# Kernel optimization log

Measured on AMD Instinct MI355X. Metric: run time of the kernel, lower is better.

## Reference

```python
import jax, jax.numpy as jnp
import numpy as np

E, N, F = 50000, 25000, 32

def setup_inputs() -> dict:
    key = jax.random.key(0)
    ks = jax.random.split(key, 8)
    efeat = jax.random.normal(ks[0], (E, F), dtype=jnp.float32) * 0.2
    initial_efeats = jax.random.normal(ks[1], (E, F), dtype=jnp.float32) * 0.2
    # msg_fn / attn_fn: Linear(F, F*F)
    Wm = jax.random.normal(ks[2], (F * F, F), dtype=jnp.float32) * 0.05
    bm = jnp.zeros((F * F,), dtype=jnp.float32)
    Wa = jax.random.normal(ks[3], (F * F, F), dtype=jnp.float32) * 0.05
    ba = jnp.zeros((F * F,), dtype=jnp.float32)
    src = jax.random.randint(ks[4], (E,), 0, N, dtype=jnp.int32)
    dst = jax.random.randint(ks[5], (E,), 0, N, dtype=jnp.int32)
    return {"efeat": efeat, "initial_efeats": initial_efeats, "Wm": Wm, "bm": bm,
            "Wa": Wa, "ba": ba, "src": src, "dst": dst, "num_nodes": N}

def reference(efeat, initial_efeats, Wm, bm, Wa, ba, src, dst, num_nodes):
    e, f = efeat.shape
    # edge-conditioned transform matrices: [E, F, F]
    w_m = (efeat @ Wm.T + bm).reshape(e, f, f)
    w_a = (efeat @ Wa.T + ba).reshape(e, f, f)
    h = efeat[:, :, None]                 # [E, F, 1]
    ih = initial_efeats[:, :, None]       # [E, F, 1]
    e1 = w_m * h                          # [E, F, F]
    exp_e2 = jnp.exp(w_a * h)             # [E, F, F]
    initial_e1 = w_m * ih
    exp_initial_e2 = jnp.exp(w_a * ih)
    # scatter-sum exp weights to destination nodes, gather back at src
    sum_exp_node = jax.ops.segment_sum(exp_e2, dst, num_segments=num_nodes)  # [N, F, F]
    sum_exp = sum_exp_node[src] - exp_e2 + exp_initial_e2
    h1 = exp_e2 * e1
    initial_h1 = exp_initial_e2 * initial_e1
    m_node = jax.ops.segment_sum(h1, dst, num_segments=num_nodes)            # [N, F, F]
    h2 = (m_node[src] - h1 + initial_h1) / sum_exp
    return h2.sum(axis=1)                 # [E, F]
```

## Files before the change

kernel.cpp:

```cpp
#include <hip/hip_runtime.h>
#include <hip/hip_fp16.h>
#include <math.h>
#include <stdint.h>


#define FDIM   32
#define NNODES 25000
#define NPB    8

typedef __attribute__((ext_vector_type(8))) short bf16x8;
typedef __attribute__((ext_vector_type(4))) float f32x4;

__device__ __forceinline__ unsigned short f2bf(float f) {
    unsigned u = __float_as_uint(f);
    return (unsigned short)((u + 0x7FFFu + ((u >> 16) & 1u)) >> 16);
}
__device__ __forceinline__ unsigned f2e5(float f) {
    unsigned short hb = __half_as_ushort(__float2half(f));
    return (unsigned)((unsigned short)((hb + 0x7Fu + ((hb >> 8) & 1u)) >> 8)) & 0xFFu;
}
__device__ __forceinline__ float e52f(unsigned b) {
    return __half2float(__ushort_as_half((unsigned short)(b << 8)));
}

__global__ __launch_bounds__(256) void zero_f4(float4* __restrict__ p, int n4) {
    int i = blockIdx.x * blockDim.x + threadIdx.x;
    int stride = gridDim.x * blockDim.x;
    float4 z = make_float4(0.f, 0.f, 0.f, 0.f);
    for (; i < n4; i += stride) p[i] = z;
}

__global__ __launch_bounds__(256) void k_hist(
    const int* __restrict__ src, const int* __restrict__ dst,
    int* __restrict__ cnt_src, int* __restrict__ cnt_dst, int E) {
    int e = blockIdx.x * blockDim.x + threadIdx.x;
    if (e < E) {
        atomicAdd(&cnt_dst[dst[e]], 1);
        atomicAdd(&cnt_src[src[e]], 1);
    }
}

__global__ __launch_bounds__(256) void k_scan2(
    const int* __restrict__ cnt_dst, int* __restrict__ off_dst, int* __restrict__ cur_dst,
    const int* __restrict__ cnt_src, int* __restrict__ off_src, int* __restrict__ cur_src,
    int n) {
    const int* cnt = blockIdx.x ? cnt_src : cnt_dst;
    int* off = blockIdx.x ? off_src : off_dst;
    int* cur = blockIdx.x ? cur_src : cur_dst;
    __shared__ int wsum[4];
    __shared__ int carry_sh;
    const int tid = threadIdx.x, lane = tid & 63, w = tid >> 6;
    if (tid == 0) carry_sh = 0;
    __syncthreads();
    for (int base = 0; base < n; base += 1024) {
        int i0 = base + tid * 4;
        int v0 = (i0 + 0 < n) ? cnt[i0 + 0] : 0;
        int v1 = (i0 + 1 < n) ? cnt[i0 + 1] : 0;
        int v2 = (i0 + 2 < n) ? cnt[i0 + 2] : 0;
        int v3 = (i0 + 3 < n) ? cnt[i0 + 3] : 0;
        int s = v0 + v1 + v2 + v3;
        int inc = s;
        for (int d = 1; d < 64; d <<= 1) {
            int t = __shfl_up(inc, d, 64);
            if (lane >= d) inc += t;
        }
        if (lane == 63) wsum[w] = inc;
        __syncthreads();
        int wbase = 0;
        for (int k = 0; k < w; ++k) wbase += wsum[k];
        int carry = carry_sh;
        int excl = carry + wbase + inc - s;
        if (i0 + 0 < n) { off[i0 + 0] = excl; cur[i0 + 0] = excl; } excl += v0;
        if (i0 + 1 < n) { off[i0 + 1] = excl; cur[i0 + 1] = excl; } excl += v1;
        if (i0 + 2 < n) { off[i0 + 2] = excl; cur[i0 + 2] = excl; } excl += v2;
        if (i0 + 3 < n) { off[i0 + 3] = excl; cur[i0 + 3] = excl; }
        __syncthreads();
        if (tid == 255) carry_sh = carry + wbase + inc;
    }
    __syncthreads();
    if (tid == 0) off[n] = carry_sh;
}

__global__ __launch_bounds__(256) void k_scatter(
    const int* __restrict__ src, const int* __restrict__ dst,
    int* __restrict__ cur_src, int* __restrict__ cur_dst,
    int* __restrict__ eb_src, int* __restrict__ eb_dst, int E) {
    int e = blockIdx.x * blockDim.x + threadIdx.x;
    if (e < E) {
        int p = atomicAdd(&cur_dst[dst[e]], 1); eb_dst[p] = e;
        int q = atomicAdd(&cur_src[src[e]], 1); eb_src[q] = e;
    }
}

__global__ __launch_bounds__(256) void prep_w(
    const float* __restrict__ Wm, const float* __restrict__ Wa,
    short* __restrict__ wbuf) {
    int idx = blockIdx.x * blockDim.x + threadIdx.x;
    if (idx >= 2 * 64 * 64) return;
    int mat  = idx >> 12;
    int jt   = (idx >> 6) & 63;
    int lane = idx & 63;
    const float* W = mat ? Wa : Wm;
    const float* s = W + (size_t)(jt * 16 + (lane & 15)) * FDIM + (lane >> 4) * 8;
    bf16x8 v;
#pragma unroll
    for (int t = 0; t < 8; ++t) v[t] = (short)f2bf(s[t]);
    *(bf16x8*)(wbuf + (size_t)idx * 8) = v;
}

__global__ __launch_bounds__(256) void gemm(
    const float* __restrict__ efeat,
    const float* __restrict__ bm, const float* __restrict__ ba,
    const short* __restrict__ wbuf,
    unsigned short* __restrict__ buf, int E)
{
    const int lane = threadIdx.x & 63;
    const int wid  = threadIdx.x >> 6;
    const int et   = blockIdx.x * 4 + wid;
    if (et * 16 >= E) return;
    const int r16 = lane & 15;
    const int kq  = lane >> 4;

    const float* xa = efeat + (size_t)(et * 16 + r16) * FDIM + kq * 8;
    bf16x8 afrag;
#pragma unroll
    for (int t = 0; t < 8; ++t) afrag[t] = (short)f2bf(xa[t]);

    for (int jt = 0; jt < 64; ++jt) {
        bf16x8 bfm = *(const bf16x8*)(wbuf + ((size_t)(jt)      * 64 + lane) * 8);
        bf16x8 bfa = *(const bf16x8*)(wbuf + ((size_t)(64 + jt) * 64 + lane) * 8);
        const int j = jt * 16 + r16;
        const float biasm = bm[j], biasa = ba[j];
        f32x4 accm = {biasm, biasm, biasm, biasm};
        f32x4 acca = {biasa, biasa, biasa, biasa};
        accm = __builtin_amdgcn_mfma_f32_16x16x32_bf16(afrag, bfm, accm, 0, 0, 0);
        acca = __builtin_amdgcn_mfma_f32_16x16x32_bf16(afrag, bfa, acca, 0, 0, 0);
#pragma unroll
        for (int r = 0; r < 4; ++r) {
            int e = et * 16 + kq * 4 + r;
            unsigned pk = f2e5(accm[r]) | (f2e5(acca[r]) << 8);
            buf[(size_t)e * 1024 + j] = (unsigned short)pk;
        }
    }
}

__global__ __launch_bounds__(256) void consume(
    const float* __restrict__ efeat, const float* __restrict__ ifeat,
    const unsigned short* __restrict__ buf,
    const int* __restrict__ off_dst, const int* __restrict__ eb_dst,
    const int* __restrict__ off_src, const int* __restrict__ eb_src,
    float* __restrict__ out)
{
    __shared__ float red[2][4][32];
    const int tid = threadIdx.x;
    const int jj  = tid & 31;
    const int wv  = tid >> 6;
    int par = 0;

    const int n0 = blockIdx.x * NPB;
    const int n1 = min(NNODES, n0 + NPB);
    for (int n = n0; n < n1; ++n) {
        float S[4] = {0.f, 0.f, 0.f, 0.f};
        float M[4] = {0.f, 0.f, 0.f, 0.f};
        const int a0 = off_dst[n], a1 = off_dst[n + 1];
        for (int idx = a0; idx < a1; ++idx) {
            int e = __builtin_amdgcn_readfirstlane(eb_dst[idx]);
            const unsigned short* bp = buf + (size_t)e * 1024 + tid;
            const float* xv = efeat + e * FDIM;
#pragma unroll
            for (int q = 0; q < 4; ++q) {
                unsigned p = bp[q * 256];
                float am = e52f(p & 0xFF), aa = e52f(p >> 8);
                float xi = xv[(q * 256 + tid) >> 5];
                float e2 = __expf(aa * xi);
                S[q] += e2;
                M[q] = fmaf(e2, am * xi, M[q]);
            }
        }
        const int b0 = off_src[n], b1 = off_src[n + 1];
        for (int idx = b0; idx < b1; ++idx) {
            int e = __builtin_amdgcn_readfirstlane(eb_src[idx]);
            const unsigned short* bp = buf + (size_t)e * 1024 + tid;
            const float* xv  = efeat + e * FDIM;
            const float* x0v = ifeat + e * FDIM;
            float acc = 0.f;
#pragma unroll
            for (int q = 0; q < 4; ++q) {
                unsigned p = bp[q * 256];
                float am = e52f(p & 0xFF), aa = e52f(p >> 8);
                int ii = (q * 256 + tid) >> 5;
                float xi = xv[ii], x0i = x0v[ii];
                float e2  = __expf(aa * xi);
                float h1  = e2 * (am * xi);
                float ei2 = __expf(aa * x0i);
                float ih1 = ei2 * (am * x0i);
                float den = (S[q] - e2) + ei2;
                float num = (M[q] - h1) + ih1;
                float h2  = num * __builtin_amdgcn_rcpf(den);
                if (!isfinite(h2)) h2 = 0.f;
                acc += h2;
            }
            acc += __shfl_xor(acc, 32, 64);
            if ((tid & 32) == 0) red[par][wv][jj] = acc;
            __syncthreads();
            if (tid < 32) {
                float s = red[par][0][tid] + red[par][1][tid]
                        + red[par][2][tid] + red[par][3][tid];
                out[(size_t)e * FDIM + tid] = s;
            }
            par ^= 1;
        }
    }
}

extern "C" void kernel_launch(void* const* d_in, const int* in_sizes, int n_in,
                              void* d_out, int out_size, void* d_ws, size_t ws_size,
                              hipStream_t stream) {
    const float* efeat = (const float*)d_in[0];
    const float* ifeat = (const float*)d_in[1];
    const float* Wm    = (const float*)d_in[2];
    const float* bm    = (const float*)d_in[3];
    const float* Wa    = (const float*)d_in[4];
    const float* ba    = (const float*)d_in[5];
    const int*   src   = (const int*)d_in[6];
    const int*   dst   = (const int*)d_in[7];
    const int E = in_sizes[6];
    const int N = NNODES;
    float* out = (float*)d_out;

    int* cnt_dst = (int*)d_ws;
    int* cnt_src = cnt_dst + N;
    int* off_dst = cnt_src + N;
    int* off_src = off_dst + (N + 1);
    int* cur_dst = off_src + (N + 1);
    int* cur_src = cur_dst + N;
    int* eb_dst  = cur_src + N;
    int* eb_src  = eb_dst + E;
    short* wbuf  = (short*)(((uintptr_t)(eb_src + E) + 255) & ~(uintptr_t)255);
    unsigned short* buf =
        (unsigned short*)(((uintptr_t)(wbuf + 2 * 64 * 64 * 8) + 255) & ~(uintptr_t)255);

    zero_f4<<<64, 256, 0, stream>>>((float4*)cnt_dst, (2 * N) / 4);
    k_hist<<<(E + 255) / 256, 256, 0, stream>>>(src, dst, cnt_src, cnt_dst, E);
    k_scan2<<<2, 256, 0, stream>>>(cnt_dst, off_dst, cur_dst,
                                   cnt_src, off_src, cur_src, N);
    k_scatter<<<(E + 255) / 256, 256, 0, stream>>>(src, dst, cur_src, cur_dst,
                                                   eb_src, eb_dst, E);
    prep_w<<<32, 256, 0, stream>>>(Wm, Wa, wbuf);

    const int etiles = (E + 15) / 16;
    gemm<<<(etiles + 3) / 4, 256, 0, stream>>>(efeat, bm, ba, wbuf, buf, E);
    consume<<<(N + NPB - 1) / NPB, 256, 0, stream>>>(efeat, ifeat, buf,
                                                     off_dst, eb_dst,
                                                     off_src, eb_src, out);
}
```

Measured before the change: 219.7 us.

## Vectorize consume buffer loads per thread and fold weight prep into scan kernel

The consume kernel now has each thread load four contiguous packed entries as one 8-byte read, so each thread handles a single input row i instead of striding through the 1024-entry block. The reduction over i becomes a three-step cross-lane shuffle followed by a reshaped shared-memory sum. Byte decoding is simplified to shifts and masks, and the weight-conversion kernel is merged into the scan launch as extra blocks to save one kernel launch. Together these cut load instructions and per-element index arithmetic, at the cost of more shuffles per output edge.

New measurement: 224.8 us. 1.02x slower.

```diff
diff --git a/kernel.cpp b/kernel.cpp
--- a/kernel.cpp
+++ b/kernel.cpp
@@ -19,8 +19,9 @@
     unsigned short hb = __half_as_ushort(__float2half(f));
     return (unsigned)((unsigned short)((hb + 0x7Fu + ((hb >> 8) & 1u)) >> 8)) & 0xFFu;
 }
-__device__ __forceinline__ float e52f(unsigned b) {
-    return __half2float(__ushort_as_half((unsigned short)(b << 8)));
+__device__ __forceinline__ void dec2(unsigned p, float& am, float& aa) {
+    am = __half2float(__ushort_as_half((unsigned short)(p << 8)));
+    aa = __half2float(__ushort_as_half((unsigned short)(p & 0xFF00u)));
 }
 
 __global__ __launch_bounds__(256) void zero_f4(float4* __restrict__ p, int n4) {
@@ -40,10 +41,27 @@
     }
 }
 
-__global__ __launch_bounds__(256) void k_scan2(
+__global__ __launch_bounds__(256) void k_scan2_prep(
     const int* __restrict__ cnt_dst, int* __restrict__ off_dst, int* __restrict__ cur_dst,
     const int* __restrict__ cnt_src, int* __restrict__ off_src, int* __restrict__ cur_src,
-    int n) {
+    int n,
+    const float* __restrict__ Wm, const float* __restrict__ Wa,
+    short* __restrict__ wbuf)
+{
+    if (blockIdx.x >= 2) {
+        int idx = (blockIdx.x - 2) * blockDim.x + threadIdx.x;
+        if (idx >= 2 * 64 * 64) return;
+        int mat  = idx >> 12;
+        int jt   = (idx >> 6) & 63;
+        int lane = idx & 63;
+        const float* W = mat ? Wa : Wm;
+        const float* s = W + (size_t)(jt * 16 + (lane & 15)) * FDIM + (lane >> 4) * 8;
+        bf16x8 v;
+#pragma unroll
+        for (int t = 0; t < 8; ++t) v[t] = (short)f2bf(s[t]);
+        *(bf16x8*)(wbuf + (size_t)idx * 8) = v;
+        return;
+    }
     const int* cnt = blockIdx.x ? cnt_src : cnt_dst;
     int* off = blockIdx.x ? off_src : off_dst;
     int* cur = blockIdx.x ? cur_src : cur_dst;
@@ -92,22 +110,6 @@
     }
 }
 
-__global__ __launch_bounds__(256) void prep_w(
-    const float* __restrict__ Wm, const float* __restrict__ Wa,
-    short* __restrict__ wbuf) {
-    int idx = blockIdx.x * blockDim.x + threadIdx.x;
-    if (idx >= 2 * 64 * 64) return;
-    int mat  = idx >> 12;
-    int jt   = (idx >> 6) & 63;
-    int lane = idx & 63;
-    const float* W = mat ? Wa : Wm;
-    const float* s = W + (size_t)(jt * 16 + (lane & 15)) * FDIM + (lane >> 4) * 8;
-    bf16x8 v;
-#pragma unroll
-    for (int t = 0; t < 8; ++t) v[t] = (short)f2bf(s[t]);
-    *(bf16x8*)(wbuf + (size_t)idx * 8) = v;
-}
-
 __global__ __launch_bounds__(256) void gemm(
     const float* __restrict__ efeat,
     const float* __restrict__ bm, const float* __restrict__ ba,
@@ -151,10 +153,11 @@
     const int* __restrict__ off_src, const int* __restrict__ eb_src,
     float* __restrict__ out)
 {
-    __shared__ float red[2][4][32];
+    __shared__ float red[2][4][8][4];
     const int tid = threadIdx.x;
-    const int jj  = tid & 31;
+    const int iidx = tid >> 3;
     const int wv  = tid >> 6;
+    const int lb  = tid & 63;
     int par = 0;
 
     const int n0 = blockIdx.x * NPB;
@@ -165,13 +168,13 @@
         const int a0 = off_dst[n], a1 = off_dst[n + 1];
         for (int idx = a0; idx < a1; ++idx) {
             int e = __builtin_amdgcn_readfirstlane(eb_dst[idx]);
-            const unsigned short* bp = buf + (size_t)e * 1024 + tid;
-            const float* xv = efeat + e * FDIM;
+            uint2 pv = *(const uint2*)(buf + (size_t)e * 1024 + 4 * tid);
+            float xi = efeat[e * FDIM + iidx];
+            unsigned pq[4] = {pv.x & 0xFFFFu, pv.x >> 16,
+                              pv.y & 0xFFFFu, pv.y >> 16};
 #pragma unroll
             for (int q = 0; q < 4; ++q) {
-                unsigned p = bp[q * 256];
-                float am = e52f(p & 0xFF), aa = e52f(p >> 8);
-                float xi = xv[(q * 256 + tid) >> 5];
+                float am, aa; dec2(pq[q], am, aa);
                 float e2 = __expf(aa * xi);
                 S[q] += e2;
                 M[q] = fmaf(e2, am * xi, M[q]);
@@ -180,16 +183,15 @@
         const int b0 = off_src[n], b1 = off_src[n + 1];
         for (int idx = b0; idx < b1; ++idx) {
             int e = __builtin_amdgcn_readfirstlane(eb_src[idx]);
-            const unsigned short* bp = buf + (size_t)e * 1024 + tid;
-            const float* xv  = efeat + e * FDIM;
-            const float* x0v = ifeat + e * FDIM;
-            float acc = 0.f;
+            uint2 pv = *(const uint2*)(buf + (size_t)e * 1024 + 4 * tid);
+            float xi  = efeat[e * FDIM + iidx];
+            float x0i = ifeat[e * FDIM + iidx];
+            unsigned pq[4] = {pv.x & 0xFFFFu, pv.x >> 16,
+                              pv.y & 0xFFFFu, pv.y >> 16};
+            float acc[4];
 #pragma unroll
             for (int q = 0; q < 4; ++q) {
-                unsigned p = bp[q * 256];
-                float am = e52f(p & 0xFF), aa = e52f(p >> 8);
-                int ii = (q * 256 + tid) >> 5;
-                float xi = xv[ii], x0i = x0v[ii];
+                float am, aa; dec2(pq[q], am, aa);
                 float e2  = __expf(aa * xi);
                 float h1  = e2 * (am * xi);
                 float ei2 = __expf(aa * x0i);
@@ -198,14 +200,22 @@
                 float num = (M[q] - h1) + ih1;
                 float h2  = num * __builtin_amdgcn_rcpf(den);
                 if (!isfinite(h2)) h2 = 0.f;
-                acc += h2;
-            }
-            acc += __shfl_xor(acc, 32, 64);
-            if ((tid & 32) == 0) red[par][wv][jj] = acc;
+                acc[q] = h2;
+            }
+#pragma unroll
+            for (int q = 0; q < 4; ++q) {
+                acc[q] += __shfl_xor(acc[q], 8, 64);
+                acc[q] += __shfl_xor(acc[q], 16, 64);
+                acc[q] += __shfl_xor(acc[q], 32, 64);
+            }
+            if (lb < 8)
+                *(float4*)&red[par][wv][lb][0] =
+                    make_float4(acc[0], acc[1], acc[2], acc[3]);
             __syncthreads();
             if (tid < 32) {
-                float s = red[par][0][tid] + red[par][1][tid]
-                        + red[par][2][tid] + red[par][3][tid];
+                int bb = tid >> 2, q = tid & 3;
+                float s = red[par][0][bb][q] + red[par][1][bb][q]
+                        + red[par][2][bb][q] + red[par][3][bb][q];
                 out[(size_t)e * FDIM + tid] = s;
             }
             par ^= 1;
@@ -242,11 +252,11 @@
 
     zero_f4<<<64, 256, 0, stream>>>((float4*)cnt_dst, (2 * N) / 4);
     k_hist<<<(E + 255) / 256, 256, 0, stream>>>(src, dst, cnt_src, cnt_dst, E);
-    k_scan2<<<2, 256, 0, stream>>>(cnt_dst, off_dst, cur_dst,
-                                   cnt_src, off_src, cur_src, N);
+    k_scan2_prep<<<34, 256, 0, stream>>>(cnt_dst, off_dst, cur_dst,
+                                         cnt_src, off_src, cur_src, N,
+                                         Wm, Wa, wbuf);
     k_scatter<<<(E + 255) / 256, 256, 0, stream>>>(src, dst, cur_src, cur_dst,
                                                    eb_src, eb_dst, E);
-    prep_w<<<32, 256, 0, stream>>>(Wm, Wa, wbuf);
 
     const int etiles = (E + 15) / 16;
     gemm<<<(etiles + 3) / 4, 256, 0, stream>>>(efeat, bm, ba, wbuf, buf, E);
```

## Transpose GEMM output for vectorized stores, fuse weight prep into scan kernel

Applied to the files above, without the earlier changes.

The GEMM now swaps the MFMA operands so each lane holds four consecutive output columns for one edge. That lets each lane write a single 8-byte packed store instead of four scattered 2-byte stores. Each block handles one 16-edge tile, with its four waves splitting the 64 column tiles. FP8-style packing now uses the hardware packed half conversion (round toward zero) plus a byte permute, which changes rounding slightly. The weight-prep kernel is merged into the scan launch as extra blocks, removing one launch.

Measured after the change: 235.9 us. 7.4% more time.

```diff
diff --git a/kernel.cpp b/kernel.cpp
--- a/kernel.cpp
+++ b/kernel.cpp
@@ -15,12 +15,15 @@
     unsigned u = __float_as_uint(f);
     return (unsigned short)((u + 0x7FFFu + ((u >> 16) & 1u)) >> 16);
 }
-__device__ __forceinline__ unsigned f2e5(float f) {
-    unsigned short hb = __half_as_ushort(__float2half(f));
-    return (unsigned)((unsigned short)((hb + 0x7Fu + ((hb >> 8) & 1u)) >> 8)) & 0xFFu;
-}
-__device__ __forceinline__ float e52f(unsigned b) {
-    return __half2float(__ushort_as_half((unsigned short)(b << 8)));
+__device__ __forceinline__ unsigned short pack_e5(float am, float aa) {
+    auto hp = __builtin_amdgcn_cvt_pkrtz(am, aa);
+    unsigned u;
+    __builtin_memcpy(&u, &hp, 4);
+    return (unsigned short)__builtin_amdgcn_perm(0u, u, 0x0301u);
+}
+__device__ __forceinline__ void dec2(unsigned v, float& am, float& aa) {
+    am = __half2float(__ushort_as_half((unsigned short)((v & 0xFFu) << 8)));
+    aa = __half2float(__ushort_as_half((unsigned short)(v & 0xFF00u)));
 }
 
 __global__ __launch_bounds__(256) void zero_f4(float4* __restrict__ p, int n4) {
@@ -40,10 +43,27 @@
     }
 }
 
-__global__ __launch_bounds__(256) void k_scan2(
+__global__ __launch_bounds__(256) void k_scan2_prep(
     const int* __restrict__ cnt_dst, int* __restrict__ off_dst, int* __restrict__ cur_dst,
     const int* __restrict__ cnt_src, int* __restrict__ off_src, int* __restrict__ cur_src,
-    int n) {
+    int n,
+    const float* __restrict__ Wm, const float* __restrict__ Wa,
+    short* __restrict__ wbuf)
+{
+    if (blockIdx.x >= 2) {
+        int idx = (blockIdx.x - 2) * blockDim.x + threadIdx.x;
+        if (idx >= 2 * 64 * 64) return;
+        int mat  = idx >> 12;
+        int jt   = (idx >> 6) & 63;
+        int lane = idx & 63;
+        const float* W = mat ? Wa : Wm;
+        const float* s = W + (size_t)(jt * 16 + (lane & 15)) * FDIM + (lane >> 4) * 8;
+        bf16x8 v;
+#pragma unroll
+        for (int t = 0; t < 8; ++t) v[t] = (short)f2bf(s[t]);
+        *(bf16x8*)(wbuf + (size_t)idx * 8) = v;
+        return;
+    }
     const int* cnt = blockIdx.x ? cnt_src : cnt_dst;
     int* off = blockIdx.x ? off_src : off_dst;
     int* cur = blockIdx.x ? cur_src : cur_dst;
@@ -92,22 +112,6 @@
     }
 }
 
-__global__ __launch_bounds__(256) void prep_w(
-    const float* __restrict__ Wm, const float* __restrict__ Wa,
-    short* __restrict__ wbuf) {
-    int idx = blockIdx.x * blockDim.x + threadIdx.x;
-    if (idx >= 2 * 64 * 64) return;
-    int mat  = idx >> 12;
-    int jt   = (idx >> 6) & 63;
-    int lane = idx & 63;
-    const float* W = mat ? Wa : Wm;
-    const float* s = W + (size_t)(jt * 16 + (lane & 15)) * FDIM + (lane >> 4) * 8;
-    bf16x8 v;
-#pragma unroll
-    for (int t = 0; t < 8; ++t) v[t] = (short)f2bf(s[t]);
-    *(bf16x8*)(wbuf + (size_t)idx * 8) = v;
-}
-
 __global__ __launch_bounds__(256) void gemm(
     const float* __restrict__ efeat,
     const float* __restrict__ bm, const float* __restrict__ ba,
@@ -116,31 +120,35 @@
 {
     const int lane = threadIdx.x & 63;
     const int wid  = threadIdx.x >> 6;
-    const int et   = blockIdx.x * 4 + wid;
+    const int et   = blockIdx.x;
     if (et * 16 >= E) return;
-    const int r16 = lane & 15;
-    const int kq  = lane >> 4;
-
-    const float* xa = efeat + (size_t)(et * 16 + r16) * FDIM + kq * 8;
-    bf16x8 afrag;
-#pragma unroll
-    for (int t = 0; t < 8; ++t) afrag[t] = (short)f2bf(xa[t]);
-
-    for (int jt = 0; jt < 64; ++jt) {
-        bf16x8 bfm = *(const bf16x8*)(wbuf + ((size_t)(jt)      * 64 + lane) * 8);
-        bf16x8 bfa = *(const bf16x8*)(wbuf + ((size_t)(64 + jt) * 64 + lane) * 8);
-        const int j = jt * 16 + r16;
-        const float biasm = bm[j], biasa = ba[j];
-        f32x4 accm = {biasm, biasm, biasm, biasm};
-        f32x4 acca = {biasa, biasa, biasa, biasa};
-        accm = __builtin_amdgcn_mfma_f32_16x16x32_bf16(afrag, bfm, accm, 0, 0, 0);
-        acca = __builtin_amdgcn_mfma_f32_16x16x32_bf16(afrag, bfa, acca, 0, 0, 0);
-#pragma unroll
-        for (int r = 0; r < 4; ++r) {
-            int e = et * 16 + kq * 4 + r;
-            unsigned pk = f2e5(accm[r]) | (f2e5(acca[r]) << 8);
-            buf[(size_t)e * 1024 + j] = (unsigned short)pk;
-        }
+    const int r16  = lane & 15;
+    const int quad = lane >> 4;
+
+    const float* xa = efeat + (size_t)(et * 16 + r16) * FDIM + quad * 8;
+    bf16x8 efrag;
+#pragma unroll
+    for (int t = 0; t < 8; ++t) efrag[t] = (short)f2bf(xa[t]);
+
+    unsigned short* brow = buf + (size_t)(et * 16 + r16) * 1024 + quad * 4;
+
+    const int jt0 = wid * 16;
+#pragma unroll 4
+    for (int jt = jt0; jt < jt0 + 16; ++jt) {
+        bf16x8 wm = *(const bf16x8*)(wbuf + ((size_t)(jt)      * 64 + lane) * 8);
+        bf16x8 wa = *(const bf16x8*)(wbuf + ((size_t)(64 + jt) * 64 + lane) * 8);
+        float4 bmv = *(const float4*)(bm + jt * 16 + quad * 4);
+        float4 bav = *(const float4*)(ba + jt * 16 + quad * 4);
+        f32x4 accm = {bmv.x, bmv.y, bmv.z, bmv.w};
+        f32x4 acca = {bav.x, bav.y, bav.z, bav.w};
+        accm = __builtin_amdgcn_mfma_f32_16x16x32_bf16(wm, efrag, accm, 0, 0, 0);
+        acca = __builtin_amdgcn_mfma_f32_16x16x32_bf16(wa, efrag, acca, 0, 0, 0);
+        unsigned lo = (unsigned)pack_e5(accm[0], acca[0])
+                    | ((unsigned)pack_e5(accm[1], acca[1]) << 16);
+        unsigned hi = (unsigned)pack_e5(accm[2], acca[2])
+                    | ((unsigned)pack_e5(accm[3], acca[3]) << 16);
+        uint2 pk = {lo, hi};
+        *(uint2*)(brow + jt * 16) = pk;
     }
 }
 
@@ -170,7 +178,7 @@
 #pragma unroll
             for (int q = 0; q < 4; ++q) {
                 unsigned p = bp[q * 256];
-                float am = e52f(p & 0xFF), aa = e52f(p >> 8);
+                float am, aa; dec2(p, am, aa);
                 float xi = xv[(q * 256 + tid) >> 5];
                 float e2 = __expf(aa * xi);
                 S[q] += e2;
@@ -187,7 +195,7 @@
 #pragma unroll
             for (int q = 0; q < 4; ++q) {
                 unsigned p = bp[q * 256];
-                float am = e52f(p & 0xFF), aa = e52f(p >> 8);
+                float am, aa; dec2(p, am, aa);
                 int ii = (q * 256 + tid) >> 5;
                 float xi = xv[ii], x0i = x0v[ii];
                 float e2  = __expf(aa * xi);
@@ -242,14 +250,14 @@
 
     zero_f4<<<64, 256, 0, stream>>>((float4*)cnt_dst, (2 * N) / 4);
     k_hist<<<(E + 255) / 256, 256, 0, stream>>>(src, dst, cnt_src, cnt_dst, E);
-    k_scan2<<<2, 256, 0, stream>>>(cnt_dst, off_dst, cur_dst,
-                                   cnt_src, off_src, cur_src, N);
+    k_scan2_prep<<<34, 256, 0, stream>>>(cnt_dst, off_dst, cur_dst,
+                                         cnt_src, off_src, cur_src, N,
+                                         Wm, Wa, wbuf);
     k_scatter<<<(E + 255) / 256, 256, 0, stream>>>(src, dst, cur_src, cur_dst,
                                                    eb_src, eb_dst, E);
-    prep_w<<<32, 256, 0, stream>>>(Wm, Wa, wbuf);
 
     const int etiles = (E + 15) / 16;
-    gemm<<<(etiles + 3) / 4, 256, 0, stream>>>(efeat, bm, ba, wbuf, buf, E);
+    gemm<<<etiles, 256, 0, stream>>>(efeat, bm, ba, wbuf, buf, E);
     consume<<<(N + NPB - 1) / NPB, 256, 0, stream>>>(efeat, ifeat, buf,
                                                      off_dst, eb_dst,
                                                      off_src, eb_src, out);
```
